# Optimization experiments

Hardware: AMD Instinct MI355X
Metric: run time of the kernel (lower is better)

The kernel has to match this reference:

```python
import jax, jax.numpy as jnp
import numpy as np

T, C, H = 8192, 2048, 8
D = C // H  # head_dim = 256
SCALE = D ** -0.5


def setup_inputs() -> dict:
    key = jax.random.key(0)
    ks = jax.random.split(key, 10)
    s = C ** -0.5  # Linear default init scale-ish
    return {
        "x": jax.random.normal(ks[0], (T, C), jnp.float32),
        "y": jax.random.normal(ks[1], (T, C), jnp.float32),
        "Wq": jax.random.normal(ks[2], (C, C), jnp.float32) * s,
        "bq": jax.random.normal(ks[3], (C,), jnp.float32) * s,
        "Wk": jax.random.normal(ks[4], (C, C), jnp.float32) * s,
        "bk": jax.random.normal(ks[5], (C,), jnp.float32) * s,
        "Wv": jax.random.normal(ks[6], (C, C), jnp.float32) * s,
        "bv": jax.random.normal(ks[7], (C,), jnp.float32) * s,
        "Wo": jax.random.normal(ks[8], (C, C), jnp.float32) * s,
        "bo": jax.random.normal(ks[9], (C,), jnp.float32) * s,
    }


def reference(x, y, Wq, bq, Wk, bk, Wv, bv, Wo, bo):
    # Linears (torch Linear: x @ W.T + b), then view [T, H, D]
    q = (x @ Wq.T + bq).reshape(T, H, D)
    k = (y @ Wk.T + bk).reshape(T, H, D)
    v = (y @ Wv.T + bv).reshape(T, H, D)
    # Faithful to source: T is the batch dim of the matmul, so attention is
    # a per-token [H, H] matrix across heads, NOT token-token attention.
    scores = jnp.einsum("thd,tgd->thg", q, k) * SCALE  # [T, H, H]
    attn = jax.nn.softmax(scores, axis=-1)
    out = jnp.einsum("thg,tgd->thd", attn, v).reshape(T, C)
    out = out @ Wo.T + bo
    return out + x
```

## Files before the change

kernel.cpp:

```cpp
#include <hip/hip_runtime.h>
#include <cstdint>
#include <cstddef>

#define T_TOK 8192
#define C_DIM 2048
#define H_HEADS 8
#define D_HEAD 256

typedef __bf16 v8bf __attribute__((ext_vector_type(8)));
typedef float v4f __attribute__((ext_vector_type(4)));
typedef float v8f __attribute__((ext_vector_type(8)));

__device__ __forceinline__ void async_load16(const void* gptr, void* lptr) {
    auto g = reinterpret_cast<__attribute__((address_space(1))) void*>(
        reinterpret_cast<uintptr_t>(gptr));
    auto l = reinterpret_cast<__attribute__((address_space(3))) void*>(
        static_cast<uint32_t>(reinterpret_cast<uintptr_t>(lptr)));
    __builtin_amdgcn_global_load_lds(g, l, 16, 0, 0);
}

__global__ __launch_bounds__(256) void cvt_kernel(
    const float* __restrict__ in, __bf16* __restrict__ out)
{
    const size_t i = ((size_t)blockIdx.x * 256 + threadIdx.x) * 8;
    v8f f = *(const v8f*)&in[i];
    v8bf b;
#pragma unroll
    for (int j = 0; j < 8; ++j) b[j] = (__bf16)f[j];
    *(v8bf*)&out[i] = b;
}

template <typename OutT>
__global__ __launch_bounds__(512, 2) void gemm256_kernel(
    const __bf16* __restrict__ A, const __bf16* __restrict__ B,
    const float* __restrict__ bias, const float* __restrict__ residual,
    OutT* __restrict__ Cmat, int M, int N, int K)
{
    __shared__ __align__(16) __bf16 lds_a[2][256 * 64];
    __shared__ __align__(16) __bf16 lds_b[2][256 * 64];

    const int tid  = threadIdx.x;
    const int wave = tid >> 6;
    const int lane = tid & 63;
    const int lane_m = lane & 15;
    const int quad   = lane >> 4;

    const int nbm = M >> 8;
    const int nbn = N >> 8;
    const int npx = nbn >> 3;
    const int bb   = blockIdx.x;
    const int xcd  = bb & 7;
    const int slot = bb >> 3;
    const int n_blk = xcd * npx + slot / nbm;
    const int m_blk = slot % nbm;
    const int block_m = m_blk << 8;
    const int block_n = n_blk << 8;

    const int wave_m = wave >> 2;
    const int wave_n = wave & 3;

    const __bf16* aSrc[4];
    const __bf16* bSrc[4];
    int ldsOff[4];
#pragma unroll
    for (int r = 0; r < 4; ++r) {
        const int li  = r * 512 + tid;
        const int row = li >> 3;
        const int p   = li & 7;
        const int c   = (p - row) & 7;
        aSrc[r] = &A[(size_t)(block_m + row) * K + c * 8];
        bSrc[r] = &B[(size_t)(block_n + row) * K + c * 8];
        ldsOff[r] = (r * 512 + wave * 64) * 8;
    }

    auto stage = [&](int buf, int kt) {
#pragma unroll
        for (int r = 0; r < 4; ++r) {
            async_load16(aSrc[r] + kt, &lds_a[buf][ldsOff[r]]);
            async_load16(bSrc[r] + kt, &lds_b[buf][ldsOff[r]]);
        }
    };

    v4f acc[8][4];
#pragma unroll
    for (int i = 0; i < 8; ++i)
#pragma unroll
        for (int j = 0; j < 4; ++j) {
            acc[i][j][0] = 0.f; acc[i][j][1] = 0.f;
            acc[i][j][2] = 0.f; acc[i][j][3] = 0.f;
        }

    stage(0, 0);
    stage(1, 64);
    asm volatile("s_waitcnt vmcnt(8)" ::: "memory");
    __builtin_amdgcn_s_barrier();

    const int NT = K >> 6;
    int cur = 0;
    for (int t = 0; t < NT; ++t) {
        const int kt2 = (t + 2) << 6;
#pragma unroll
        for (int kk = 0; kk < 2; ++kk) {
            v8bf af[8], bfr[4];
#pragma unroll
            for (int i = 0; i < 8; ++i) {
                const int r = wave_m * 128 + i * 16 + lane_m;
                const int p = (kk * 4 + quad + r) & 7;
                af[i] = *(const v8bf*)&lds_a[cur][r * 64 + p * 8];
            }
#pragma unroll
            for (int j = 0; j < 4; ++j) {
                const int r = wave_n * 64 + j * 16 + lane_m;
                const int p = (kk * 4 + quad + r) & 7;
                bfr[j] = *(const v8bf*)&lds_b[cur][r * 64 + p * 8];
            }
            if (kk == 1) {
                asm volatile("s_waitcnt lgkmcnt(0)" ::: "memory");
                __builtin_amdgcn_s_barrier();
                if (t + 2 < NT) stage(cur, kt2);
            }
            __builtin_amdgcn_s_setprio(1);
#pragma unroll
            for (int i = 0; i < 8; ++i)
#pragma unroll
                for (int j = 0; j < 4; ++j)
                    acc[i][j] = __builtin_amdgcn_mfma_f32_16x16x32_bf16(
                        af[i], bfr[j], acc[i][j], 0, 0, 0);
            __builtin_amdgcn_s_setprio(0);
        }
        if (t < NT - 1) {
            if (t + 2 < NT) {
                asm volatile("s_waitcnt vmcnt(8)" ::: "memory");
            } else {
                asm volatile("s_waitcnt vmcnt(0)" ::: "memory");
            }
            __builtin_amdgcn_s_barrier();
        }
        cur ^= 1;
    }

#pragma unroll
    for (int i = 0; i < 8; ++i) {
        const int row0 = block_m + wave_m * 128 + i * 16 + quad * 4;
#pragma unroll
        for (int j = 0; j < 4; ++j) {
            const int col = block_n + wave_n * 64 + j * 16 + lane_m;
            const float bv = bias[col];
#pragma unroll
            for (int r = 0; r < 4; ++r) {
                float val = acc[i][j][r] + bv;
                const size_t off = (size_t)(row0 + r) * N + col;
                if (residual) val += residual[off];
                Cmat[off] = (OutT)val;
            }
        }
    }
}

__global__ __launch_bounds__(256) void attn_kernel(
    const __bf16* __restrict__ q, const __bf16* __restrict__ kv,
    __bf16* __restrict__ out)
{
    __shared__ __align__(16) __bf16 sq[4 * 2048];
    __shared__ __align__(16) __bf16 sk[4 * 2048];
    __shared__ __align__(16) __bf16 sv[4 * 2048];

    const int wave = threadIdx.x >> 6;
    const int lane = threadIdx.x & 63;
    const int t = blockIdx.x * 4 + wave;

    const __bf16* qt = q + (size_t)t * C_DIM;
    const __bf16* kt = kv + (size_t)t * 2 * C_DIM;
    const __bf16* vt = kt + C_DIM;
    __bf16* sqw = &sq[wave * C_DIM];
    __bf16* skw = &sk[wave * C_DIM];
    __bf16* svw = &sv[wave * C_DIM];

#pragma unroll
    for (int p = 0; p < 4; ++p) {
        const int idx = (p * 64 + lane) * 8;
        *(v8bf*)&sqw[idx] = *(const v8bf*)&qt[idx];
        *(v8bf*)&skw[idx] = *(const v8bf*)&kt[idx];
        *(v8bf*)&svw[idx] = *(const v8bf*)&vt[idx];
    }

    const int h = lane >> 3;
    const int g = lane & 7;
    float s = 0.f;
#pragma unroll 4
    for (int d = 0; d < D_HEAD; d += 8) {
        v8bf qa = *(const v8bf*)&sqw[h * D_HEAD + d];
        v8bf ka = *(const v8bf*)&skw[g * D_HEAD + d];
#pragma unroll
        for (int jj = 0; jj < 8; ++jj) s += (float)qa[jj] * (float)ka[jj];
    }
    s *= 0.0625f;

    float m = s;
    m = fmaxf(m, __shfl_xor(m, 1));
    m = fmaxf(m, __shfl_xor(m, 2));
    m = fmaxf(m, __shfl_xor(m, 4));
    const float e = __expf(s - m);
    float dsum = e;
    dsum += __shfl_xor(dsum, 1);
    dsum += __shfl_xor(dsum, 2);
    dsum += __shfl_xor(dsum, 4);
    const float p_attn = e / dsum;

    float attnv[8];
#pragma unroll
    for (int gg = 0; gg < 8; ++gg)
        attnv[gg] = __shfl(p_attn, (lane & 56) | gg);

    __bf16* outp = out + (size_t)t * C_DIM + h * D_HEAD + g * 32;
    const __bf16* vbase = &svw[g * 32];
#pragma unroll
    for (int dd = 0; dd < 32; dd += 8) {
        float o[8] = {0.f, 0.f, 0.f, 0.f, 0.f, 0.f, 0.f, 0.f};
#pragma unroll
        for (int gg = 0; gg < 8; ++gg) {
            v8bf vv = *(const v8bf*)&vbase[gg * D_HEAD + dd];
            const float pg = attnv[gg];
#pragma unroll
            for (int jj = 0; jj < 8; ++jj) o[jj] += pg * (float)vv[jj];
        }
        v8bf ov;
#pragma unroll
        for (int jj = 0; jj < 8; ++jj) ov[jj] = (__bf16)o[jj];
        *(v8bf*)&outp[dd] = ov;
    }
}

extern "C" void kernel_launch(void* const* d_in, const int* in_sizes, int n_in,
                              void* d_out, int out_size, void* d_ws, size_t ws_size,
                              hipStream_t stream) {
    const float* x  = (const float*)d_in[0];
    const float* y  = (const float*)d_in[1];
    const float* Wq = (const float*)d_in[2];
    const float* bq = (const float*)d_in[3];
    const float* Wk = (const float*)d_in[4];
    const float* bk = (const float*)d_in[5];
    const float* Wv = (const float*)d_in[6];
    const float* bv = (const float*)d_in[7];
    const float* Wo = (const float*)d_in[8];
    const float* bo = (const float*)d_in[9];
    float* out = (float*)d_out;

    const size_t TC = (size_t)T_TOK * C_DIM;
    const size_t CC = (size_t)C_DIM * C_DIM;

    __bf16* xb    = (__bf16*)d_ws;
    __bf16* kv_ws = xb;
    __bf16* yb    = xb + 2 * TC;
    __bf16* q_ws  = yb + TC;
    __bf16* Wb    = q_ws + TC;
    float*  bias_kv = (float*)(Wb + 2 * CC);
    __bf16* a_ws  = q_ws;

    dim3 cblock(256), gblock(512);
    const dim3 cvtTC(TC / (8 * 256)), cvtCC(CC / (8 * 256));

    cvt_kernel<<<cvtTC, cblock, 0, stream>>>(x, xb);
    cvt_kernel<<<cvtTC, cblock, 0, stream>>>(y, yb);
    hipMemcpyAsync(bias_kv,        bk, C_DIM * sizeof(float),
                   hipMemcpyDeviceToDevice, stream);
    hipMemcpyAsync(bias_kv + C_DIM, bv, C_DIM * sizeof(float),
                   hipMemcpyDeviceToDevice, stream);

    cvt_kernel<<<cvtCC, cblock, 0, stream>>>(Wq, Wb);
    gemm256_kernel<__bf16><<<dim3((T_TOK/256)*(C_DIM/256)), gblock, 0, stream>>>(
        xb, Wb, bq, nullptr, q_ws, T_TOK, C_DIM, C_DIM);

    cvt_kernel<<<cvtCC, cblock, 0, stream>>>(Wk, Wb);
    cvt_kernel<<<cvtCC, cblock, 0, stream>>>(Wv, Wb + CC);
    gemm256_kernel<__bf16><<<dim3((T_TOK/256)*(2*C_DIM/256)), gblock, 0, stream>>>(
        yb, Wb, bias_kv, nullptr, kv_ws, T_TOK, 2 * C_DIM, C_DIM);

    attn_kernel<<<dim3(T_TOK / 4), cblock, 0, stream>>>(q_ws, kv_ws, a_ws);

    cvt_kernel<<<cvtCC, cblock, 0, stream>>>(Wo, Wb);
    gemm256_kernel<float><<<dim3((T_TOK/256)*(C_DIM/256)), gblock, 0, stream>>>(
        a_ws, Wb, bo, x, out, T_TOK, C_DIM, C_DIM);
}
```

Measured before the change: 569.4 us.

## Split GEMM K-tile into four MFMA phases interleaved with staggered async loads

Restructures the GEMM main loop into four quadrant phases (A-half × B-half). Each phase reads its own fragments from LDS and issues a slice of the next tile's global-to-LDS loads, with barriers between phases. The aim is to spread memory traffic across the tile and overlap it with MFMA work instead of issuing all loads at once, which also cuts live fragment registers. The extra barriers per iteration and the finer-grained vmcnt accounting add sync overhead and correctness risk.

```diff
diff --git a/kernel.cpp b/kernel.cpp
--- a/kernel.cpp
+++ b/kernel.cpp
@@ -59,26 +59,19 @@
     const int wave_m = wave >> 2;
     const int wave_n = wave & 3;
 
-    const __bf16* aSrc[4];
-    const __bf16* bSrc[4];
-    int ldsOff[4];
-#pragma unroll
-    for (int r = 0; r < 4; ++r) {
-        const int li  = r * 512 + tid;
-        const int row = li >> 3;
-        const int p   = li & 7;
-        const int c   = (p - row) & 7;
-        aSrc[r] = &A[(size_t)(block_m + row) * K + c * 8];
-        bSrc[r] = &B[(size_t)(block_n + row) * K + c * 8];
-        ldsOff[r] = (r * 512 + wave * 64) * 8;
-    }
-
-    auto stage = [&](int buf, int kt) {
-#pragma unroll
-        for (int r = 0; r < 4; ++r) {
-            async_load16(aSrc[r] + kt, &lds_a[buf][ldsOff[r]]);
-            async_load16(bSrc[r] + kt, &lds_b[buf][ldsOff[r]]);
-        }
+    const int srow = tid >> 3;
+    const int crot = ((tid & 7) - srow) & 7;
+    const __bf16* aRow0 = &A[(size_t)(block_m + srow) * K + crot * 8];
+    const __bf16* bRow0 = &B[(size_t)(block_n + srow) * K + crot * 8];
+    const int ldsW = wave * 512;
+
+    auto stA = [&](int buf, int kt, int r) {
+        async_load16(aRow0 + ((size_t)r * 64 * K + kt),
+                     &lds_a[buf][r * 4096 + ldsW]);
+    };
+    auto stB = [&](int buf, int kt, int r) {
+        async_load16(bRow0 + ((size_t)r * 64 * K + kt),
+                     &lds_b[buf][r * 4096 + ldsW]);
     };
 
     v4f acc[8][4];
@@ -90,54 +83,102 @@
             acc[i][j][2] = 0.f; acc[i][j][3] = 0.f;
         }
 
-    stage(0, 0);
-    stage(1, 64);
-    asm volatile("s_waitcnt vmcnt(8)" ::: "memory");
+    const int NT = K >> 6;
+    stA(0, 0, 0); stA(0, 0, 2); stA(0, 0, 1); stA(0, 0, 3);
+    stB(0, 0, 0); stB(0, 0, 1); stB(0, 0, 2); stB(0, 0, 3);
+    if (NT > 1) {
+        stA(1, 64, 0); stA(1, 64, 2);
+        asm volatile("s_waitcnt vmcnt(2)" ::: "memory");
+    } else {
+        asm volatile("s_waitcnt vmcnt(0)" ::: "memory");
+    }
     __builtin_amdgcn_s_barrier();
 
-    const int NT = K >> 6;
-    int cur = 0;
+#define PHASE_MFMA(IA, JB)                                                   \
+    __builtin_amdgcn_s_setprio(1);                                           \
+    _Pragma("unroll") for (int kk = 0; kk < 2; ++kk)                         \
+    _Pragma("unroll") for (int i = 0; i < 4; ++i)                            \
+    _Pragma("unroll") for (int j = 0; j < 2; ++j)                            \
+        acc[(IA)*4 + i][(JB)*2 + j] =                                        \
+            __builtin_amdgcn_mfma_f32_16x16x32_bf16(                         \
+                af[kk][i], bfr[JB][kk][j], acc[(IA)*4 + i][(JB)*2 + j],      \
+                0, 0, 0);                                                    \
+    __builtin_amdgcn_s_setprio(0);
+
+#define PHASE_SYNC_IN                                                        \
+    __builtin_amdgcn_sched_barrier(0);                                       \
+    __builtin_amdgcn_s_barrier();                                            \
+    asm volatile("s_waitcnt lgkmcnt(0)" ::: "memory");                       \
+    __builtin_amdgcn_sched_barrier(0);
+
     for (int t = 0; t < NT; ++t) {
+        const int cur = t & 1;
+        const int nxt = cur ^ 1;
+        const int kt1 = (t + 1) << 6;
         const int kt2 = (t + 2) << 6;
-#pragma unroll
-        for (int kk = 0; kk < 2; ++kk) {
-            v8bf af[8], bfr[4];
-#pragma unroll
-            for (int i = 0; i < 8; ++i) {
+        v8bf af[2][4], bfr[2][2][2];
+
+#pragma unroll
+        for (int kk = 0; kk < 2; ++kk)
+#pragma unroll
+            for (int i = 0; i < 4; ++i) {
                 const int r = wave_m * 128 + i * 16 + lane_m;
                 const int p = (kk * 4 + quad + r) & 7;
-                af[i] = *(const v8bf*)&lds_a[cur][r * 64 + p * 8];
-            }
-#pragma unroll
-            for (int j = 0; j < 4; ++j) {
+                af[kk][i] = *(const v8bf*)&lds_a[cur][r * 64 + p * 8];
+            }
+#pragma unroll
+        for (int kk = 0; kk < 2; ++kk)
+#pragma unroll
+            for (int j = 0; j < 2; ++j) {
                 const int r = wave_n * 64 + j * 16 + lane_m;
                 const int p = (kk * 4 + quad + r) & 7;
-                bfr[j] = *(const v8bf*)&lds_b[cur][r * 64 + p * 8];
-            }
-            if (kk == 1) {
-                asm volatile("s_waitcnt lgkmcnt(0)" ::: "memory");
-                __builtin_amdgcn_s_barrier();
-                if (t + 2 < NT) stage(cur, kt2);
-            }
-            __builtin_amdgcn_s_setprio(1);
-#pragma unroll
-            for (int i = 0; i < 8; ++i)
-#pragma unroll
-                for (int j = 0; j < 4; ++j)
-                    acc[i][j] = __builtin_amdgcn_mfma_f32_16x16x32_bf16(
-                        af[i], bfr[j], acc[i][j], 0, 0, 0);
-            __builtin_amdgcn_s_setprio(0);
-        }
+                bfr[0][kk][j] = *(const v8bf*)&lds_b[cur][r * 64 + p * 8];
+            }
+        if (t + 1 < NT) { stA(nxt, kt1, 1); stA(nxt, kt1, 3); }
+        PHASE_SYNC_IN
+        PHASE_MFMA(0, 0)
+        __builtin_amdgcn_s_barrier();
+
+#pragma unroll
+        for (int kk = 0; kk < 2; ++kk)
+#pragma unroll
+            for (int j = 0; j < 2; ++j) {
+                const int r = wave_n * 64 + (2 + j) * 16 + lane_m;
+                const int p = (kk * 4 + quad + r) & 7;
+                bfr[1][kk][j] = *(const v8bf*)&lds_b[cur][r * 64 + p * 8];
+            }
+        if (t + 1 < NT) { stB(nxt, kt1, 0); stB(nxt, kt1, 1); }
+        PHASE_SYNC_IN
+        PHASE_MFMA(0, 1)
+        __builtin_amdgcn_s_barrier();
+
+#pragma unroll
+        for (int kk = 0; kk < 2; ++kk)
+#pragma unroll
+            for (int i = 0; i < 4; ++i) {
+                const int r = wave_m * 128 + (4 + i) * 16 + lane_m;
+                const int p = (kk * 4 + quad + r) & 7;
+                af[kk][i] = *(const v8bf*)&lds_a[cur][r * 64 + p * 8];
+            }
+        if (t + 1 < NT) { stB(nxt, kt1, 2); stB(nxt, kt1, 3); }
+        PHASE_SYNC_IN
+        PHASE_MFMA(1, 1)
+        __builtin_amdgcn_s_barrier();
+
+        if (t + 2 < NT) { stA(cur, kt2, 0); stA(cur, kt2, 2); }
+        PHASE_SYNC_IN
+        PHASE_MFMA(1, 0)
         if (t < NT - 1) {
             if (t + 2 < NT) {
-                asm volatile("s_waitcnt vmcnt(8)" ::: "memory");
+                asm volatile("s_waitcnt vmcnt(2)" ::: "memory");
             } else {
                 asm volatile("s_waitcnt vmcnt(0)" ::: "memory");
             }
             __builtin_amdgcn_s_barrier();
         }
-        cur ^= 1;
-    }
+    }
+#undef PHASE_MFMA
+#undef PHASE_SYNC_IN
 
 #pragma unroll
     for (int i = 0; i < 8; ++i) {
```

Result: slower. 584.6 us (+2.7%).

## Restructure GEMM mainloop into four-stage ring of K=32 slices with split staging

Applied to the files above, without the earlier changes.

The GEMM replaces its double-buffered K=64 LDS tiles with a four-slot ring of K=32 slices. The swizzle changes from 8 to 4 chunks per row, and prefetch runs three slices ahead. Each iteration splits its MFMA work into two halves over the A rows, and each half issues half of the next slice's async loads, so global-to-LDS traffic interleaves more finely with compute. The cost is more barriers per unit of K and fewer MFMAs between syncs, which could offset the deeper prefetch.

```diff
diff --git a/kernel.cpp b/kernel.cpp
--- a/kernel.cpp
+++ b/kernel.cpp
@@ -36,8 +36,7 @@
     const float* __restrict__ bias, const float* __restrict__ residual,
     OutT* __restrict__ Cmat, int M, int N, int K)
 {
-    __shared__ __align__(16) __bf16 lds_a[2][256 * 64];
-    __shared__ __align__(16) __bf16 lds_b[2][256 * 64];
+    __shared__ __align__(16) __bf16 lds[4 * 16384];
 
     const int tid  = threadIdx.x;
     const int wave = tid >> 6;
@@ -59,27 +58,29 @@
     const int wave_m = wave >> 2;
     const int wave_n = wave & 3;
 
-    const __bf16* aSrc[4];
-    const __bf16* bSrc[4];
-    int ldsOff[4];
-#pragma unroll
-    for (int r = 0; r < 4; ++r) {
-        const int li  = r * 512 + tid;
-        const int row = li >> 3;
-        const int p   = li & 7;
-        const int c   = (p - row) & 7;
-        aSrc[r] = &A[(size_t)(block_m + row) * K + c * 8];
-        bSrc[r] = &B[(size_t)(block_n + row) * K + c * 8];
-        ldsOff[r] = (r * 512 + wave * 64) * 8;
-    }
-
-    auto stage = [&](int buf, int kt) {
-#pragma unroll
-        for (int r = 0; r < 4; ++r) {
-            async_load16(aSrc[r] + kt, &lds_a[buf][ldsOff[r]]);
-            async_load16(bSrc[r] + kt, &lds_b[buf][ldsOff[r]]);
-        }
+    const int srow4 = tid >> 2;
+    const int crot  = ((tid & 3) - (tid >> 2)) & 3;
+    const __bf16* aS = &A[(size_t)(block_m + srow4) * K + crot * 8];
+    const __bf16* bS = &B[(size_t)(block_n + srow4) * K + crot * 8];
+    const int dstW = wave * 512;
+
+    auto stg = [&](int s, int h, int l) {
+        const size_t go = (size_t)l * 128 * K + (size_t)h * 32;
+        async_load16(aS + go, &lds[s * 16384 +        l * 4096 + dstW]);
+        async_load16(bS + go, &lds[s * 16384 + 8192 + l * 4096 + dstW]);
     };
+
+    int aOff[8], bOff[4];
+#pragma unroll
+    for (int i = 0; i < 8; ++i) {
+        const int r = wave_m * 128 + i * 16 + lane_m;
+        aOff[i] = r * 32 + ((quad + r) & 3) * 8;
+    }
+#pragma unroll
+    for (int j = 0; j < 4; ++j) {
+        const int r = wave_n * 64 + j * 16 + lane_m;
+        bOff[j] = 8192 + r * 32 + ((quad + r) & 3) * 8;
+    }
 
     v4f acc[8][4];
 #pragma unroll
@@ -90,53 +91,63 @@
             acc[i][j][2] = 0.f; acc[i][j][3] = 0.f;
         }
 
-    stage(0, 0);
-    stage(1, 64);
+    const int NH = K >> 5;
+    stg(0, 0, 0); stg(0, 0, 1);
+    stg(1, 1, 0); stg(1, 1, 1);
+    stg(2, 2, 0); stg(2, 2, 1);
     asm volatile("s_waitcnt vmcnt(8)" ::: "memory");
     __builtin_amdgcn_s_barrier();
 
-    const int NT = K >> 6;
-    int cur = 0;
-    for (int t = 0; t < NT; ++t) {
-        const int kt2 = (t + 2) << 6;
-#pragma unroll
-        for (int kk = 0; kk < 2; ++kk) {
-            v8bf af[8], bfr[4];
-#pragma unroll
-            for (int i = 0; i < 8; ++i) {
-                const int r = wave_m * 128 + i * 16 + lane_m;
-                const int p = (kk * 4 + quad + r) & 7;
-                af[i] = *(const v8bf*)&lds_a[cur][r * 64 + p * 8];
-            }
-#pragma unroll
-            for (int j = 0; j < 4; ++j) {
-                const int r = wave_n * 64 + j * 16 + lane_m;
-                const int p = (kk * 4 + quad + r) & 7;
-                bfr[j] = *(const v8bf*)&lds_b[cur][r * 64 + p * 8];
-            }
-            if (kk == 1) {
-                asm volatile("s_waitcnt lgkmcnt(0)" ::: "memory");
-                __builtin_amdgcn_s_barrier();
-                if (t + 2 < NT) stage(cur, kt2);
-            }
-            __builtin_amdgcn_s_setprio(1);
-#pragma unroll
-            for (int i = 0; i < 8; ++i)
-#pragma unroll
-                for (int j = 0; j < 4; ++j)
-                    acc[i][j] = __builtin_amdgcn_mfma_f32_16x16x32_bf16(
-                        af[i], bfr[j], acc[i][j], 0, 0, 0);
-            __builtin_amdgcn_s_setprio(0);
-        }
-        if (t < NT - 1) {
-            if (t + 2 < NT) {
+    for (int h = 0; h < NH; ++h) {
+        const int sb = (h & 3) * 16384;
+        const int sp = (h + 3) & 3;
+        const bool do_stage = (h + 3 < NH);
+        v8bf bfr[4], af[4], af2[4];
+
+#pragma unroll
+        for (int j = 0; j < 4; ++j)
+            bfr[j] = *(const v8bf*)&lds[sb + bOff[j]];
+#pragma unroll
+        for (int i = 0; i < 4; ++i)
+            af[i] = *(const v8bf*)&lds[sb + aOff[i]];
+        if (do_stage) stg(sp, h + 3, 0);
+        __builtin_amdgcn_s_barrier();
+        asm volatile("s_waitcnt lgkmcnt(0)" ::: "memory");
+        __builtin_amdgcn_s_setprio(1);
+#pragma unroll
+        for (int i = 0; i < 4; ++i)
+#pragma unroll
+            for (int j = 0; j < 4; ++j)
+                acc[i][j] = __builtin_amdgcn_mfma_f32_16x16x32_bf16(
+                    af[i], bfr[j], acc[i][j], 0, 0, 0);
+        __builtin_amdgcn_s_setprio(0);
+        __builtin_amdgcn_s_barrier();
+
+#pragma unroll
+        for (int i = 0; i < 4; ++i)
+            af2[i] = *(const v8bf*)&lds[sb + aOff[4 + i]];
+        if (do_stage) stg(sp, h + 3, 1);
+        __builtin_amdgcn_s_barrier();
+        asm volatile("s_waitcnt lgkmcnt(0)" ::: "memory");
+        __builtin_amdgcn_s_setprio(1);
+#pragma unroll
+        for (int i = 0; i < 4; ++i)
+#pragma unroll
+            for (int j = 0; j < 4; ++j)
+                acc[4 + i][j] = __builtin_amdgcn_mfma_f32_16x16x32_bf16(
+                    af2[i], bfr[j], acc[4 + i][j], 0, 0, 0);
+        __builtin_amdgcn_s_setprio(0);
+
+        if (h < NH - 1) {
+            if (h + 3 < NH) {
                 asm volatile("s_waitcnt vmcnt(8)" ::: "memory");
+            } else if (h + 2 < NH) {
+                asm volatile("s_waitcnt vmcnt(4)" ::: "memory");
             } else {
                 asm volatile("s_waitcnt vmcnt(0)" ::: "memory");
             }
             __builtin_amdgcn_s_barrier();
         }
-        cur ^= 1;
     }
 
 #pragma unroll
```

Result: slower. 603.9 us (+6.1%).
